# Optimization experiments

Measured on AMD Instinct MI355X. Metric: run time of the kernel, lower is better.

Reference implementation:

```python
import jax, jax.numpy as jnp
import numpy as np

N_ATOMS = 64
D_IN = 128
H = 4
D = 32


def setup_inputs() -> dict:
    key = jax.random.key(0)
    ks = jax.random.split(key, 7)
    s = 0.05
    return {
        "pair_features": jax.random.normal(ks[0], (N_ATOMS, N_ATOMS, D_IN), jnp.float32),
        "atom_mask": jnp.ones((N_ATOMS,), jnp.int32),
        "Wq": jax.random.normal(ks[1], (D_IN, H * D), jnp.float32) * s,
        "bq": jnp.zeros((H * D,), jnp.float32),
        "Wk": jax.random.normal(ks[2], (D_IN, H * D), jnp.float32) * s,
        "bk": jnp.zeros((H * D,), jnp.float32),
        "Wv": jax.random.normal(ks[3], (D_IN, H * D), jnp.float32) * s,
        "bv": jnp.zeros((H * D,), jnp.float32),
    }


def reference(pair_features, atom_mask, Wq, bq, Wk, bk, Wv, bv):
    n = pair_features.shape[0]
    S = n * n  # flattened pair sequence length
    x = pair_features.reshape(S, -1)  # (S, D_in)
    # QKV projections -> (H, S, D)
    q = (x @ Wq + bq).reshape(S, H, D).transpose(1, 0, 2)
    k = (x @ Wk + bk).reshape(S, H, D).transpose(1, 0, 2)
    v = (x @ Wv + bv).reshape(S, H, D).transpose(1, 0, 2)
    scale = 1.0 / float(D) ** 0.5
    # key-side validity mask over flattened pairs
    av = atom_mask.astype(bool)
    key_valid = (av[:, None] & av[None, :]).reshape(S)  # (S,)
    # attention scores (H, S, S) -- the memory-dominant intermediate
    scores = jnp.einsum('hsd,htd->hst', q, k) * scale
    neg = jnp.asarray(jnp.finfo(scores.dtype).min, scores.dtype)
    scores = jnp.where(key_valid[None, None, :], scores, neg)
    p = jax.nn.softmax(scores, axis=-1)
    out = jnp.einsum('hst,htd->hsd', p, v)  # (H, S, D)
    attn_out = out.transpose(1, 0, 2).reshape(n, n, H * D)
    # sum-pool over second atom axis
    return attn_out.sum(axis=1)  # (n_atoms, H*D)
```

## Files before the change

### kernel.cpp

```cpp
#include <hip/hip_runtime.h>
#include <hip/hip_bf16.h>

#define S_TOT 4096
#define NA 64
#define DIN 128
#define HD 128
#define NH 4
#define DH 32
#define QROWS 16
#define QSC 0.2550348564632784f

typedef __attribute__((ext_vector_type(8))) short bf16x8;
typedef __attribute__((ext_vector_type(4))) short bf16x4;
typedef __attribute__((ext_vector_type(4))) float f32x4;

#define EXP2(x) exp2f(x)

#define MFMA32(A, B, C) __builtin_amdgcn_mfma_f32_16x16x32_bf16(A, B, C, 0, 0, 0)
#define MFMA16(A, B, C) __builtin_amdgcn_mfma_f32_16x16x16bf16_1k(A, B, C, 0, 0, 0)

__device__ __forceinline__ unsigned pk_bf16(float lo, float hi) {
    return __builtin_amdgcn_perm(__builtin_bit_cast(unsigned, hi),
                                 __builtin_bit_cast(unsigned, lo), 0x07060302u);
}

__global__ __launch_bounds__(512) void qkv_kernel(
    const float* __restrict__ x,
    const float* __restrict__ Wq, const float* __restrict__ bq,
    const float* __restrict__ Wk, const float* __restrict__ bk,
    const float* __restrict__ Wv, const float* __restrict__ bv,
    __hip_bfloat16* __restrict__ Qb, __hip_bfloat16* __restrict__ Kb,
    __hip_bfloat16* __restrict__ Vt)
{
    __shared__ __hip_bfloat16 xs[QROWS][DIN + 8];
    const int tid = threadIdx.x;
    const int c  = tid & 15;
    const int g  = (tid >> 4) & 3;
    const int wv = tid >> 6;
    const int r0 = blockIdx.x * QROWS;

    {
        const int e  = tid * 4;
        const int rr = e >> 7, cc = e & 127;
        const float4 xv = *(const float4*)(x + (size_t)(r0 + rr) * DIN + cc);
        xs[rr][cc + 0] = __float2bfloat16(xv.x);
        xs[rr][cc + 1] = __float2bfloat16(xv.y);
        xs[rr][cc + 2] = __float2bfloat16(xv.z);
        xs[rr][cc + 3] = __float2bfloat16(xv.w);
    }
    __syncthreads();

    bf16x8 af[4];
    #pragma unroll
    for (int ks = 0; ks < 4; ++ks)
        af[ks] = *(const bf16x8*)&xs[c][ks * 32 + g * 8];

    #pragma unroll
    for (int t = 0; t < 3; ++t) {
        const int nt = wv * 3 + t;
        const float* W  = (nt < 8) ? Wq : (nt < 16 ? Wk : Wv);
        const float* bb = (nt < 8) ? bq : (nt < 16 ? bk : bv);
        const int n0 = (nt & 7) * 16;

        f32x4 acc = {0.f, 0.f, 0.f, 0.f};
        #pragma unroll
        for (int ks = 0; ks < 4; ++ks) {
            union { bf16x8 v; unsigned short s[8]; } bfv;
            #pragma unroll
            for (int j = 0; j < 8; ++j)
                bfv.s[j] = __builtin_bit_cast(unsigned short,
                    __float2bfloat16(W[(size_t)(ks * 32 + g * 8 + j) * HD + n0 + c]));
            acc = MFMA32(af[ks], bfv.v, acc);
        }
        const float bval = bb[n0 + c];
        if (nt < 8) {
            #pragma unroll
            for (int r = 0; r < 4; ++r)
                Qb[(size_t)(r0 + g * 4 + r) * HD + n0 + c] =
                    __float2bfloat16((acc[r] + bval) * QSC);
        } else if (nt < 16) {
            #pragma unroll
            for (int r = 0; r < 4; ++r)
                Kb[(size_t)(r0 + g * 4 + r) * HD + n0 + c] =
                    __float2bfloat16(acc[r] + bval);
        } else {
            unsigned short p[4];
            #pragma unroll
            for (int r = 0; r < 4; ++r)
                p[r] = __builtin_bit_cast(unsigned short,
                        __float2bfloat16(acc[r] + bval));
            uint2 d;
            d.x = ((unsigned)p[1] << 16) | p[0];
            d.y = ((unsigned)p[3] << 16) | p[2];
            *(uint2*)((unsigned short*)Vt + (size_t)(n0 + c) * S_TOT + r0 + g * 4) = d;
        }
    }
}

__global__ __launch_bounds__(512) void attn_kernel(
    const __hip_bfloat16* __restrict__ Qbp, const __hip_bfloat16* __restrict__ Kbp,
    const __hip_bfloat16* __restrict__ Vtp, const int* __restrict__ am,
    float* __restrict__ out)
{
    __shared__ float pO[8][64][33];
    __shared__ float pL[8][64];
    __shared__ float rinv[64];
    __shared__ float pR[16][33];
    __shared__ float amadd[64];
    __shared__ int allvS;

    const int i   = blockIdx.x;
    const int h   = blockIdx.y;
    const int tid = threadIdx.x;
    const int c   = tid & 15;
    const int g   = (tid >> 4) & 3;
    const int wv  = tid >> 6;

    if (tid < 64) {
        const int a = am[tid];
        amadd[tid] = a ? 0.f : -1e30f;
        const unsigned long long bal = __ballot(a != 0);
        if (tid == 0) allvS = (bal == ~0ull) ? 1 : 0;
    }
    __syncthreads();
    const bool allv = (allvS != 0);

    const short* Q = (const short*)Qbp;
    const short* K = (const short*)Kbp;
    const short* V = (const short*)Vtp;

    bf16x8 qf[4];
    #pragma unroll
    for (int qs = 0; qs < 4; ++qs)
        qf[qs] = *(const bf16x8*)(Q + ((size_t)(i * 64 + qs * 16 + c) * HD + h * DH + g * 8));

    f32x4 acc[2][4];
    #pragma unroll
    for (int ds = 0; ds < 2; ++ds)
        #pragma unroll
        for (int qs = 0; qs < 4; ++qs)
            acc[ds][qs] = (f32x4){0.f, 0.f, 0.f, 0.f};
    float l_run[4] = {0.f, 0.f, 0.f, 0.f};

    const int t0base = wv * 512;
    bf16x8 ka[4];
    #pragma unroll
    for (int ms = 0; ms < 4; ++ms)
        ka[ms] = *(const bf16x8*)(K + ((size_t)(t0base + ms * 16 + c) * HD + h * DH + g * 8));

    for (int kt = 0; kt < 8; ++kt) {
        const int t0 = t0base + kt * 64;

        bf16x4 va[2][4];
        #pragma unroll
        for (int ds = 0; ds < 2; ++ds)
            #pragma unroll
            for (int ks = 0; ks < 4; ++ks)
                va[ds][ks] = *(const bf16x4*)(V + ((size_t)(h * DH + ds * 16 + c) * S_TOT + t0 + ks * 16 + g * 4));

        f32x4 sc[4][4];
        #pragma unroll
        for (int ms = 0; ms < 4; ++ms)
            #pragma unroll
            for (int qs = 0; qs < 4; ++qs)
                sc[ms][qs] = MFMA32(ka[ms], qf[qs], ((f32x4){0.f, 0.f, 0.f, 0.f}));

        bf16x8 kan[4];
        if (kt < 7) {
            #pragma unroll
            for (int ms = 0; ms < 4; ++ms)
                kan[ms] = *(const bf16x8*)(K + ((size_t)(t0 + 64 + ms * 16 + c) * HD + h * DH + g * 8));
        }

        if (!allv) {
            const float tadd = am[t0 >> 6] ? 0.f : -1e30f;
            #pragma unroll
            for (int ms = 0; ms < 4; ++ms)
                #pragma unroll
                for (int r = 0; r < 4; ++r) {
                    const float a = amadd[ms * 16 + g * 4 + r] + tadd;
                    #pragma unroll
                    for (int qs = 0; qs < 4; ++qs) sc[ms][qs][r] += a;
                }
        }

        unsigned pk[4][4][2];
        #pragma unroll
        for (int qs = 0; qs < 4; ++qs) {
            float rs = 0.f;
            #pragma unroll
            for (int ms = 0; ms < 4; ++ms) {
                const float p0 = EXP2(sc[ms][qs][0]);
                const float p1 = EXP2(sc[ms][qs][1]);
                const float p2 = EXP2(sc[ms][qs][2]);
                const float p3 = EXP2(sc[ms][qs][3]);
                rs += (p0 + p1) + (p2 + p3);
                pk[ms][qs][0] = pk_bf16(p0, p1);
                pk[ms][qs][1] = pk_bf16(p2, p3);
            }
            rs += __shfl_xor(rs, 16);
            rs += __shfl_xor(rs, 32);
            l_run[qs] += rs;
        }

        #pragma unroll
        for (int ks = 0; ks < 4; ++ks)
            #pragma unroll
            for (int qs = 0; qs < 4; ++qs) {
                union { unsigned u[2]; bf16x4 v; } bb;
                bb.u[0] = pk[ks][qs][0];
                bb.u[1] = pk[ks][qs][1];
                #pragma unroll
                for (int ds = 0; ds < 2; ++ds)
                    acc[ds][qs] = MFMA16(va[ds][ks], bb.v, acc[ds][qs]);
            }

        #pragma unroll
        for (int ms = 0; ms < 4; ++ms) ka[ms] = kan[ms];
    }

    #pragma unroll
    for (int ds = 0; ds < 2; ++ds)
        #pragma unroll
        for (int qs = 0; qs < 4; ++qs)
            #pragma unroll
            for (int r = 0; r < 4; ++r)
                pO[wv][qs * 16 + c][ds * 16 + g * 4 + r] = acc[ds][qs][r];
    if (g == 0) {
        #pragma unroll
        for (int qs = 0; qs < 4; ++qs) pL[wv][qs * 16 + c] = l_run[qs];
    }
    __syncthreads();

    if (tid < 64) {
        float L = 0.f;
        #pragma unroll
        for (int w = 0; w < 8; ++w) L += pL[w][tid];
        rinv[tid] = 1.f / fmaxf(L, 1e-30f);
    }
    __syncthreads();

    {
        const int d = tid & 31, qb = tid >> 5;
        float s = 0.f;
        #pragma unroll
        for (int qq = 0; qq < 4; ++qq) {
            const int q = qb * 4 + qq;
            float o = 0.f;
            #pragma unroll
            for (int w = 0; w < 8; ++w) o += pO[w][q][d];
            s += o * rinv[q];
        }
        pR[qb][d] = s;
    }
    __syncthreads();

    if (tid < 32) {
        float o = 0.f;
        #pragma unroll
        for (int j = 0; j < 16; ++j) o += pR[j][tid];
        out[(size_t)i * HD + h * DH + tid] = o;
    }
}

extern "C" void kernel_launch(void* const* d_in, const int* in_sizes, int n_in,
                              void* d_out, int out_size, void* d_ws, size_t ws_size,
                              hipStream_t stream) {
    const float* x  = (const float*)d_in[0];
    const int*   am = (const int*)d_in[1];
    const float* Wq = (const float*)d_in[2];
    const float* bq = (const float*)d_in[3];
    const float* Wk = (const float*)d_in[4];
    const float* bk = (const float*)d_in[5];
    const float* Wv = (const float*)d_in[6];
    const float* bv = (const float*)d_in[7];
    float* outp = (float*)d_out;

    __hip_bfloat16* Qb = (__hip_bfloat16*)d_ws;
    __hip_bfloat16* Kb = Qb + (size_t)S_TOT * HD;
    __hip_bfloat16* Vt = Kb + (size_t)S_TOT * HD;

    qkv_kernel<<<S_TOT / QROWS, 512, 0, stream>>>(x, Wq, bq, Wk, bk, Wv, bv, Qb, Kb, Vt);
    attn_kernel<<<dim3(NA, NH), 512, 0, stream>>>(Qb, Kb, Vt, am, outp);
}
```

Baseline: 99.41 us.

## Split attention keys across blocks with merge kernel; pre-transpose weights to bf16

Attention now splits the key sequence into two halves across a third grid dimension, doubling the block count from 256 to 512 to fill more compute units. Per-split partial outputs and denominators go to workspace and are combined by a new merge kernel. Separately, a small kernel converts and transposes the QKV weights to bf16 once, so the projection kernel does vector loads instead of strided scalar fp32 loads. The cost is two extra kernel launches and extra global traffic for the partial results.

```diff
diff --git a/kernel.cpp b/kernel.cpp
--- a/kernel.cpp
+++ b/kernel.cpp
@@ -8,6 +8,8 @@
 #define NH 4
 #define DH 32
 #define QROWS 16
+#define KSPLIT 2
+#define KT_PER_WAVE 4
 #define QSC 0.2550348564632784f
 
 typedef __attribute__((ext_vector_type(8))) short bf16x8;
@@ -24,11 +26,35 @@
                                  __builtin_bit_cast(unsigned, lo), 0x07060302u);
 }
 
+__global__ __launch_bounds__(256) void wt_kernel(
+    const float* __restrict__ Wq, const float* __restrict__ Wk,
+    const float* __restrict__ Wv, unsigned short* __restrict__ Wt)
+{
+    __shared__ unsigned short tile[16][DIN + 8];
+    const int w  = blockIdx.x;
+    const int k0 = blockIdx.y * 16;
+    const float* W = (w == 0) ? Wq : (w == 1 ? Wk : Wv);
+    const int tid = threadIdx.x;
+    #pragma unroll
+    for (int j = 0; j < 8; ++j) {
+        const int idx = tid + j * 256;
+        const int kl = idx >> 7, n = idx & 127;
+        tile[kl][n] = __builtin_bit_cast(unsigned short,
+            __float2bfloat16(W[(size_t)(k0 + kl) * HD + n]));
+    }
+    __syncthreads();
+    #pragma unroll
+    for (int j = 0; j < 8; ++j) {
+        const int idx = tid + j * 256;
+        const int n = idx >> 4, kl = idx & 15;
+        Wt[(size_t)w * HD * DIN + (size_t)n * DIN + k0 + kl] = tile[kl][n];
+    }
+}
+
 __global__ __launch_bounds__(512) void qkv_kernel(
-    const float* __restrict__ x,
-    const float* __restrict__ Wq, const float* __restrict__ bq,
-    const float* __restrict__ Wk, const float* __restrict__ bk,
-    const float* __restrict__ Wv, const float* __restrict__ bv,
+    const float* __restrict__ x, const unsigned short* __restrict__ Wt,
+    const float* __restrict__ bq, const float* __restrict__ bk,
+    const float* __restrict__ bv,
     __hip_bfloat16* __restrict__ Qb, __hip_bfloat16* __restrict__ Kb,
     __hip_bfloat16* __restrict__ Vt)
 {
@@ -58,19 +84,16 @@
     #pragma unroll
     for (int t = 0; t < 3; ++t) {
         const int nt = wv * 3 + t;
-        const float* W  = (nt < 8) ? Wq : (nt < 16 ? Wk : Wv);
+        const int widx = (nt < 8) ? 0 : (nt < 16 ? 1 : 2);
         const float* bb = (nt < 8) ? bq : (nt < 16 ? bk : bv);
         const int n0 = (nt & 7) * 16;
+        const unsigned short* Wtw = Wt + (size_t)widx * HD * DIN;
 
         f32x4 acc = {0.f, 0.f, 0.f, 0.f};
         #pragma unroll
         for (int ks = 0; ks < 4; ++ks) {
-            union { bf16x8 v; unsigned short s[8]; } bfv;
-            #pragma unroll
-            for (int j = 0; j < 8; ++j)
-                bfv.s[j] = __builtin_bit_cast(unsigned short,
-                    __float2bfloat16(W[(size_t)(ks * 32 + g * 8 + j) * HD + n0 + c]));
-            acc = MFMA32(af[ks], bfv.v, acc);
+            const bf16x8 bfv = *(const bf16x8*)(Wtw + (size_t)(n0 + c) * DIN + ks * 32 + g * 8);
+            acc = MFMA32(af[ks], bfv, acc);
         }
         const float bval = bb[n0 + c];
         if (nt < 8) {
@@ -100,17 +123,16 @@
 __global__ __launch_bounds__(512) void attn_kernel(
     const __hip_bfloat16* __restrict__ Qbp, const __hip_bfloat16* __restrict__ Kbp,
     const __hip_bfloat16* __restrict__ Vtp, const int* __restrict__ am,
-    float* __restrict__ out)
+    float* __restrict__ Op, float* __restrict__ Lp)
 {
     __shared__ float pO[8][64][33];
     __shared__ float pL[8][64];
-    __shared__ float rinv[64];
-    __shared__ float pR[16][33];
     __shared__ float amadd[64];
     __shared__ int allvS;
 
     const int i   = blockIdx.x;
     const int h   = blockIdx.y;
+    const int z   = blockIdx.z;
     const int tid = threadIdx.x;
     const int c   = tid & 15;
     const int g   = (tid >> 4) & 3;
@@ -142,13 +164,13 @@
             acc[ds][qs] = (f32x4){0.f, 0.f, 0.f, 0.f};
     float l_run[4] = {0.f, 0.f, 0.f, 0.f};
 
-    const int t0base = wv * 512;
+    const int t0base = z * (S_TOT / KSPLIT) + wv * (KT_PER_WAVE * 64);
     bf16x8 ka[4];
     #pragma unroll
     for (int ms = 0; ms < 4; ++ms)
         ka[ms] = *(const bf16x8*)(K + ((size_t)(t0base + ms * 16 + c) * HD + h * DH + g * 8));
 
-    for (int kt = 0; kt < 8; ++kt) {
+    for (int kt = 0; kt < KT_PER_WAVE; ++kt) {
         const int t0 = t0base + kt * 64;
 
         bf16x4 va[2][4];
@@ -166,7 +188,7 @@
                 sc[ms][qs] = MFMA32(ka[ms], qf[qs], ((f32x4){0.f, 0.f, 0.f, 0.f}));
 
         bf16x8 kan[4];
-        if (kt < 7) {
+        if (kt < KT_PER_WAVE - 1) {
             #pragma unroll
             for (int ms = 0; ms < 4; ++ms)
                 kan[ms] = *(const bf16x8*)(K + ((size_t)(t0 + 64 + ms * 16 + c) * HD + h * DH + g * 8));
@@ -232,35 +254,62 @@
     }
     __syncthreads();
 
+    const int p = (i * NH + h) * KSPLIT + z;
+    {
+        const int d = tid & 31;
+        const int q0 = (tid >> 5) * 4;
+        #pragma unroll
+        for (int qq = 0; qq < 4; ++qq) {
+            const int q = q0 + qq;
+            float o = 0.f;
+            #pragma unroll
+            for (int w = 0; w < 8; ++w) o += pO[w][q][d];
+            Op[(size_t)p * (64 * DH) + q * DH + d] = o;
+        }
+    }
     if (tid < 64) {
         float L = 0.f;
         #pragma unroll
         for (int w = 0; w < 8; ++w) L += pL[w][tid];
+        Lp[(size_t)p * 64 + tid] = L;
+    }
+}
+
+__global__ __launch_bounds__(128) void merge_kernel(
+    const float* __restrict__ Op, const float* __restrict__ Lp,
+    float* __restrict__ out)
+{
+    __shared__ float rinv[64];
+    __shared__ float red[4][33];
+    const int i = blockIdx.x, h = blockIdx.y;
+    const int tid = threadIdx.x;
+    const int p0 = (i * NH + h) * KSPLIT;
+
+    if (tid < 64) {
+        float L = 0.f;
+        #pragma unroll
+        for (int zz = 0; zz < KSPLIT; ++zz) L += Lp[(size_t)(p0 + zz) * 64 + tid];
         rinv[tid] = 1.f / fmaxf(L, 1e-30f);
     }
     __syncthreads();
 
-    {
-        const int d = tid & 31, qb = tid >> 5;
-        float s = 0.f;
-        #pragma unroll
-        for (int qq = 0; qq < 4; ++qq) {
-            const int q = qb * 4 + qq;
-            float o = 0.f;
-            #pragma unroll
-            for (int w = 0; w < 8; ++w) o += pO[w][q][d];
-            s += o * rinv[q];
-        }
-        pR[qb][d] = s;
-    }
-    __syncthreads();
-
-    if (tid < 32) {
+    const int d = tid & 31, qg = tid >> 5;
+    float s = 0.f;
+    #pragma unroll 4
+    for (int qq = 0; qq < 16; ++qq) {
+        const int q = qg * 16 + qq;
         float o = 0.f;
         #pragma unroll
-        for (int j = 0; j < 16; ++j) o += pR[j][tid];
-        out[(size_t)i * HD + h * DH + tid] = o;
-    }
+        for (int zz = 0; zz < KSPLIT; ++zz)
+            o += Op[(size_t)(p0 + zz) * (64 * DH) + q * DH + d];
+        s += o * rinv[q];
+    }
+    red[qg][d] = s;
+    __syncthreads();
+
+    if (tid < 32)
+        out[(size_t)i * HD + h * DH + tid] =
+            (red[0][tid] + red[1][tid]) + (red[2][tid] + red[3][tid]);
 }
 
 extern "C" void kernel_launch(void* const* d_in, const int* in_sizes, int n_in,
@@ -268,18 +317,24 @@
                               hipStream_t stream) {
     const float* x  = (const float*)d_in[0];
     const int*   am = (const int*)d_in[1];
+    const float* bq = (const float*)d_in[3];
+    const float* bk = (const float*)d_in[5];
+    const float* bv = (const float*)d_in[7];
     const float* Wq = (const float*)d_in[2];
-    const float* bq = (const float*)d_in[3];
     const float* Wk = (const float*)d_in[4];
-    const float* bk = (const float*)d_in[5];
     const float* Wv = (const float*)d_in[6];
-    const float* bv = (const float*)d_in[7];
     float* outp = (float*)d_out;
 
-    __hip_bfloat16* Qb = (__hip_bfloat16*)d_ws;
-    __hip_bfloat16* Kb = Qb + (size_t)S_TOT * HD;
-    __hip_bfloat16* Vt = Kb + (size_t)S_TOT * HD;
-
-    qkv_kernel<<<S_TOT / QROWS, 512, 0, stream>>>(x, Wq, bq, Wk, bk, Wv, bv, Qb, Kb, Vt);
-    attn_kernel<<<dim3(NA, NH), 512, 0, stream>>>(Qb, Kb, Vt, am, outp);
-}
+    char* ws = (char*)d_ws;
+    __hip_bfloat16* Qb = (__hip_bfloat16*)(ws + 0);
+    __hip_bfloat16* Kb = (__hip_bfloat16*)(ws + (1u << 20));
+    __hip_bfloat16* Vt = (__hip_bfloat16*)(ws + (2u << 20));
+    unsigned short* Wt = (unsigned short*)(ws + (3u << 20));
+    float* Op = (float*)(ws + (4u << 20));
+    float* Lp = (float*)(ws + (9u << 20));
+
+    wt_kernel<<<dim3(3, 8), 256, 0, stream>>>(Wq, Wk, Wv, Wt);
+    qkv_kernel<<<S_TOT / QROWS, 512, 0, stream>>>(x, Wt, bq, bk, bv, Qb, Kb, Vt);
+    attn_kernel<<<dim3(NA, NH, KSPLIT), 512, 0, stream>>>(Qb, Kb, Vt, am, Op, Lp);
+    merge_kernel<<<dim3(NA, NH), 128, 0, stream>>>(Op, Lp, outp);
+}
```

Result: slower. 109.3 us (+10.0%).

## Split attention keys across blocks with atomic last-block reduction

Applied to the files above, without the earlier changes.

Splits the key dimension of the attention kernel four ways across a new grid z-dimension, using 256-thread blocks, so 1024 blocks run instead of 256 and the GPU's compute units are better occupied. Each block writes its partial output and row sums to workspace. An atomic counter picks the last block per (atom, head), and that block reduces the partials, normalises and pools. It also reorders the per-tile work to process one query subtile at a time, which lowers register pressure. The cost is an extra memset, global traffic for the partials, and a serial tail reduction.

```diff
diff --git a/kernel.cpp b/kernel.cpp
--- a/kernel.cpp
+++ b/kernel.cpp
@@ -8,6 +8,7 @@
 #define NH 4
 #define DH 32
 #define QROWS 16
+#define KSPLIT 4
 #define QSC 0.2550348564632784f
 
 typedef __attribute__((ext_vector_type(8))) short bf16x8;
@@ -97,20 +98,21 @@
     }
 }
 
-__global__ __launch_bounds__(512) void attn_kernel(
+__global__ __launch_bounds__(256, 4) void attn_kernel(
     const __hip_bfloat16* __restrict__ Qbp, const __hip_bfloat16* __restrict__ Kbp,
     const __hip_bfloat16* __restrict__ Vtp, const int* __restrict__ am,
+    float* __restrict__ Op, float* __restrict__ Lp, int* __restrict__ cnt,
     float* __restrict__ out)
 {
-    __shared__ float pO[8][64][33];
-    __shared__ float pL[8][64];
-    __shared__ float rinv[64];
-    __shared__ float pR[16][33];
+    __shared__ float pO[4][64][33];
+    __shared__ float pL[4][64];
     __shared__ float amadd[64];
-    __shared__ int allvS;
+    __shared__ float red[8][33];
+    __shared__ int allvS, lastS;
 
     const int i   = blockIdx.x;
     const int h   = blockIdx.y;
+    const int z   = blockIdx.z;
     const int tid = threadIdx.x;
     const int c   = tid & 15;
     const int g   = (tid >> 4) & 3;
@@ -142,15 +144,15 @@
             acc[ds][qs] = (f32x4){0.f, 0.f, 0.f, 0.f};
     float l_run[4] = {0.f, 0.f, 0.f, 0.f};
 
-    const int t0base = wv * 512;
-    bf16x8 ka[4];
-    #pragma unroll
-    for (int ms = 0; ms < 4; ++ms)
-        ka[ms] = *(const bf16x8*)(K + ((size_t)(t0base + ms * 16 + c) * HD + h * DH + g * 8));
-
-    for (int kt = 0; kt < 8; ++kt) {
+    const int t0base = z * (S_TOT / KSPLIT) + wv * 256;
+
+    for (int kt = 0; kt < 4; ++kt) {
         const int t0 = t0base + kt * 64;
 
+        bf16x8 ka[4];
+        #pragma unroll
+        for (int ms = 0; ms < 4; ++ms)
+            ka[ms] = *(const bf16x8*)(K + ((size_t)(t0 + ms * 16 + c) * HD + h * DH + g * 8));
         bf16x4 va[2][4];
         #pragma unroll
         for (int ds = 0; ds < 2; ++ds)
@@ -158,65 +160,49 @@
             for (int ks = 0; ks < 4; ++ks)
                 va[ds][ks] = *(const bf16x4*)(V + ((size_t)(h * DH + ds * 16 + c) * S_TOT + t0 + ks * 16 + g * 4));
 
-        f32x4 sc[4][4];
-        #pragma unroll
-        for (int ms = 0; ms < 4; ++ms)
-            #pragma unroll
-            for (int qs = 0; qs < 4; ++qs)
-                sc[ms][qs] = MFMA32(ka[ms], qf[qs], ((f32x4){0.f, 0.f, 0.f, 0.f}));
-
-        bf16x8 kan[4];
-        if (kt < 7) {
+        const float tadd = allv ? 0.f : (am[t0 >> 6] ? 0.f : -1e30f);
+
+        #pragma unroll
+        for (int qs = 0; qs < 4; ++qs) {
+            f32x4 sc[4];
             #pragma unroll
             for (int ms = 0; ms < 4; ++ms)
-                kan[ms] = *(const bf16x8*)(K + ((size_t)(t0 + 64 + ms * 16 + c) * HD + h * DH + g * 8));
-        }
-
-        if (!allv) {
-            const float tadd = am[t0 >> 6] ? 0.f : -1e30f;
-            #pragma unroll
-            for (int ms = 0; ms < 4; ++ms)
+                sc[ms] = MFMA32(ka[ms], qf[qs], ((f32x4){0.f, 0.f, 0.f, 0.f}));
+
+            if (!allv) {
                 #pragma unroll
-                for (int r = 0; r < 4; ++r) {
-                    const float a = amadd[ms * 16 + g * 4 + r] + tadd;
+                for (int ms = 0; ms < 4; ++ms)
                     #pragma unroll
-                    for (int qs = 0; qs < 4; ++qs) sc[ms][qs][r] += a;
-                }
-        }
-
-        unsigned pk[4][4][2];
-        #pragma unroll
-        for (int qs = 0; qs < 4; ++qs) {
+                    for (int r = 0; r < 4; ++r)
+                        sc[ms][r] += amadd[ms * 16 + g * 4 + r] + tadd;
+            }
+
+            unsigned pkv[4][2];
             float rs = 0.f;
             #pragma unroll
             for (int ms = 0; ms < 4; ++ms) {
-                const float p0 = EXP2(sc[ms][qs][0]);
-                const float p1 = EXP2(sc[ms][qs][1]);
-                const float p2 = EXP2(sc[ms][qs][2]);
-                const float p3 = EXP2(sc[ms][qs][3]);
+                const float p0 = EXP2(sc[ms][0]);
+                const float p1 = EXP2(sc[ms][1]);
+                const float p2 = EXP2(sc[ms][2]);
+                const float p3 = EXP2(sc[ms][3]);
                 rs += (p0 + p1) + (p2 + p3);
-                pk[ms][qs][0] = pk_bf16(p0, p1);
-                pk[ms][qs][1] = pk_bf16(p2, p3);
+                pkv[ms][0] = pk_bf16(p0, p1);
+                pkv[ms][1] = pk_bf16(p2, p3);
             }
             rs += __shfl_xor(rs, 16);
             rs += __shfl_xor(rs, 32);
             l_run[qs] += rs;
-        }
-
-        #pragma unroll
-        for (int ks = 0; ks < 4; ++ks)
-            #pragma unroll
-            for (int qs = 0; qs < 4; ++qs) {
+
+            #pragma unroll
+            for (int ks = 0; ks < 4; ++ks) {
                 union { unsigned u[2]; bf16x4 v; } bb;
-                bb.u[0] = pk[ks][qs][0];
-                bb.u[1] = pk[ks][qs][1];
+                bb.u[0] = pkv[ks][0];
+                bb.u[1] = pkv[ks][1];
                 #pragma unroll
                 for (int ds = 0; ds < 2; ++ds)
                     acc[ds][qs] = MFMA16(va[ds][ks], bb.v, acc[ds][qs]);
             }
-
-        #pragma unroll
-        for (int ms = 0; ms < 4; ++ms) ka[ms] = kan[ms];
+        }
     }
 
     #pragma unroll
@@ -232,33 +218,57 @@
     }
     __syncthreads();
 
+    const int p = (i * NH + h) * KSPLIT + z;
+    {
+        const int d = tid & 31, q0 = (tid >> 5) * 8;
+        #pragma unroll
+        for (int qq = 0; qq < 8; ++qq) {
+            const int q = q0 + qq;
+            Op[(size_t)p * (64 * DH) + q * DH + d] =
+                (pO[0][q][d] + pO[1][q][d]) + (pO[2][q][d] + pO[3][q][d]);
+        }
+    }
+    if (tid < 64)
+        Lp[(size_t)p * 64 + tid] =
+            (pL[0][tid] + pL[1][tid]) + (pL[2][tid] + pL[3][tid]);
+
+    __threadfence();
+    __syncthreads();
+    if (tid == 0)
+        lastS = (atomicAdd(&cnt[i * NH + h], 1) == KSPLIT - 1) ? 1 : 0;
+    __syncthreads();
+    if (!lastS) return;
+
+    __threadfence();
+    const int p0 = (i * NH + h) * KSPLIT;
     if (tid < 64) {
         float L = 0.f;
         #pragma unroll
-        for (int w = 0; w < 8; ++w) L += pL[w][tid];
-        rinv[tid] = 1.f / fmaxf(L, 1e-30f);
+        for (int zz = 0; zz < KSPLIT; ++zz) L += Lp[(size_t)(p0 + zz) * 64 + tid];
+        amadd[tid] = 1.f / fmaxf(L, 1e-30f);
     }
     __syncthreads();
 
     {
-        const int d = tid & 31, qb = tid >> 5;
+        const int d = tid & 31, qg = tid >> 5;
         float s = 0.f;
         #pragma unroll
-        for (int qq = 0; qq < 4; ++qq) {
-            const int q = qb * 4 + qq;
+        for (int qq = 0; qq < 8; ++qq) {
+            const int q = qg * 8 + qq;
             float o = 0.f;
             #pragma unroll
-            for (int w = 0; w < 8; ++w) o += pO[w][q][d];
-            s += o * rinv[q];
-        }
-        pR[qb][d] = s;
+            for (int zz = 0; zz < KSPLIT; ++zz)
+                o += Op[(size_t)(p0 + zz) * (64 * DH) + q * DH + d];
+            s += o * amadd[q];
+        }
+        red[qg][d] = s;
     }
     __syncthreads();
 
     if (tid < 32) {
         float o = 0.f;
         #pragma unroll
-        for (int j = 0; j < 16; ++j) o += pR[j][tid];
+        for (int j = 0; j < 8; ++j) o += red[j][tid];
         out[(size_t)i * HD + h * DH + tid] = o;
     }
 }
@@ -276,10 +286,15 @@
     const float* bv = (const float*)d_in[7];
     float* outp = (float*)d_out;
 
-    __hip_bfloat16* Qb = (__hip_bfloat16*)d_ws;
-    __hip_bfloat16* Kb = Qb + (size_t)S_TOT * HD;
-    __hip_bfloat16* Vt = Kb + (size_t)S_TOT * HD;
-
+    char* ws = (char*)d_ws;
+    __hip_bfloat16* Qb = (__hip_bfloat16*)(ws + 0);
+    __hip_bfloat16* Kb = (__hip_bfloat16*)(ws + (1u << 20));
+    __hip_bfloat16* Vt = (__hip_bfloat16*)(ws + (2u << 20));
+    float* Op  = (float*)(ws + (4u << 20));
+    float* Lp  = (float*)(ws + (13u << 20));
+    int*   cnt = (int*)(ws + (14u << 20));
+
+    hipMemsetAsync(cnt, 0, NA * NH * sizeof(int), stream);
     qkv_kernel<<<S_TOT / QROWS, 512, 0, stream>>>(x, Wq, bq, Wk, bk, Wv, bv, Qb, Kb, Vt);
-    attn_kernel<<<dim3(NA, NH), 512, 0, stream>>>(Qb, Kb, Vt, am, outp);
+    attn_kernel<<<dim3(NA, NH, KSPLIT), 256, 0, stream>>>(Qb, Kb, Vt, am, Op, Lp, cnt, outp);
 }
```

Measured after the change: 230.7 us. 132% more time.
